# Kernel tuning notes

Measured on AMD Instinct MI355X. Metric: run time of the kernel, lower is better.

## Reference

```python
import jax, jax.numpy as jnp
import numpy as np

N = 100000        # nodes
E = 1_600_000     # edges (avg degree 16)
F_IN = 128        # in_channels
HID = 64          # hidden_channels (per-head)
H1 = 4            # heads layer 1
G = 128           # number of graphs
NEG_SLOPE = 0.2   # PyG GATConv default leaky_relu slope


def setup_inputs() -> dict:
    key = jax.random.key(0)
    ks = jax.random.split(key, 12)
    x = jax.random.normal(ks[0], (N, F_IN), dtype=jnp.float32)
    edge_index = jax.random.randint(ks[1], (2, E), 0, N, dtype=jnp.int64)
    batch = jnp.sort(jax.random.randint(ks[2], (N,), 0, G, dtype=jnp.int64))
    s1 = 1.0 / np.sqrt(F_IN)
    s2 = 1.0 / np.sqrt(H1 * HID)
    # layer 1: in=F_IN, out=H1*HID (PyG lin has no bias; separate bias after concat)
    w1 = jax.random.normal(ks[3], (H1 * HID, F_IN), dtype=jnp.float32) * s1
    a_src1 = jax.random.normal(ks[4], (H1, HID), dtype=jnp.float32) * s1
    a_dst1 = jax.random.normal(ks[5], (H1, HID), dtype=jnp.float32) * s1
    b1 = jnp.zeros((H1 * HID,), dtype=jnp.float32)
    # layer 2: in=H1*HID, out=HID, heads=1
    w2 = jax.random.normal(ks[6], (1 * HID, H1 * HID), dtype=jnp.float32) * s2
    a_src2 = jax.random.normal(ks[7], (1, HID), dtype=jnp.float32) * s2
    a_dst2 = jax.random.normal(ks[8], (1, HID), dtype=jnp.float32) * s2
    b2 = jnp.zeros((HID,), dtype=jnp.float32)
    return {"x": x, "w1": w1, "a_src1": a_src1, "a_dst1": a_dst1, "b1": b1,
            "w2": w2, "a_src2": a_src2, "a_dst2": a_dst2, "b2": b2,
            "edge_index": edge_index, "batch": batch}


def _segment_softmax(alpha, seg, n):
    # numerically-stable softmax of alpha [E,H] grouped by seg (dst node)
    m = jax.ops.segment_max(alpha, seg, num_segments=n)
    m = jnp.where(jnp.isfinite(m), m, 0.0)  # empty segments -> 0
    a = jnp.exp(alpha - m[seg])
    s = jax.ops.segment_sum(a, seg, num_segments=n)
    return a / (s[seg] + 1e-16)


def _gat_conv(x, w, a_src, a_dst, bias, src, dst, n, heads, ch):
    h = (x @ w.T).reshape(n, heads, ch)          # [N,H,C]
    alpha_src = jnp.sum(h * a_src[None], axis=-1)  # [N,H]
    alpha_dst = jnp.sum(h * a_dst[None], axis=-1)  # [N,H]
    e = jax.nn.leaky_relu(alpha_src[src] + alpha_dst[dst], NEG_SLOPE)  # [E,H]
    att = _segment_softmax(e, dst, n)             # [E,H]
    msg = h[src] * att[:, :, None]                # [E,H,C]
    out = jax.ops.segment_sum(msg, dst, num_segments=n)  # [N,H,C]
    return out.reshape(n, heads * ch) + bias


def reference(x, w1, a_src1, a_dst1, b1, w2, a_src2, a_dst2, b2, edge_index, batch):
    src, dst = edge_index[0], edge_index[1]
    h = jax.nn.relu(_gat_conv(x, w1, a_src1, a_dst1, b1, src, dst, N, H1, HID))
    h = jax.nn.relu(_gat_conv(h, w2, a_src2, a_dst2, b2, src, dst, N, 1, HID))
    # global_mean_pool over graph ids
    sums = jax.ops.segment_sum(h, batch, num_segments=G)            # [G,HID]
    cnt = jax.ops.segment_sum(jnp.ones((N,), h.dtype), batch, num_segments=G)
    return sums / jnp.maximum(cnt, 1.0)[:, None]
```

## Files before the change

### kernel.cpp

```cpp
#include <hip/hip_runtime.h>
#include <math.h>
#include <type_traits>

#define NNODES 100000
#define NEDGES 1600000
#define NGRAPH 128
#define NBKT 391
#define CAP 1536
#define EPB 2048

typedef _Float16 f16x4 __attribute__((ext_vector_type(4)));
typedef _Float16 f16x8 __attribute__((ext_vector_type(8)));
typedef float f32x4 __attribute__((ext_vector_type(4)));

__global__ void convert_w(const float* __restrict__ w1, const float* __restrict__ w2,
                          const float* __restrict__ as1c, const float* __restrict__ ad1c,
                          const float* __restrict__ as2c, const float* __restrict__ ad2c,
                          _Float16* __restrict__ w1h, _Float16* __restrict__ w2h,
                          _Float16* __restrict__ va1, _Float16* __restrict__ va2) {
  const int b = blockIdx.x, tid = threadIdx.x;
  if (b < 8) {
    if (tid >= 128) return;
    int h = b & 3;
    const float* coef = (b >= 4) ? ad1c : as1c;
    float s = 0.f;
    for (int c = 0; c < 64; ++c) s = fmaf(w1[(size_t)(h * 64 + c) * 128 + tid], coef[h * 64 + c], s);
    va1[b * 128 + tid] = (_Float16)s;
  } else if (b < 10) {
    int r = b - 8;
    const float* coef = r ? ad2c : as2c;
    float s = 0.f;
    for (int c = 0; c < 64; ++c) s = fmaf(w2[(size_t)c * 256 + tid], coef[c], s);
    va2[r * 256 + tid] = (_Float16)s;
  } else if (b < 138) {
    int i = (b - 10) * 256 + tid;
    w1h[i] = (_Float16)w1[i];
  } else {
    int i = (b - 138) * 256 + tid;
    w2h[i] = (_Float16)w2[i];
  }
}

template <int K, int N, typename AT>
__global__ __launch_bounds__(256) void gemm_mfma(const AT* __restrict__ A,
    const _Float16* __restrict__ Bh, const _Float16* __restrict__ VA,
    _Float16* __restrict__ C, int M, float* __restrict__ asrc, float* __restrict__ adst) {
  constexpr int H = N / 64;
  constexpr int KS = K / 32, NT = N / 16;
  constexpr int BM = 400, NG = 7;
  constexpr int CP = N + 8;
  __shared__ _Float16 Bs[N * K];
  __shared__ _Float16 VAs[16 * K];
  __shared__ _Float16 Cs[64 * CP];
  const int tid = threadIdx.x;
  const int lane = tid & 63, wid = tid >> 6;
  const int lr = lane & 15, lk = (lane >> 4) * 8;
  const int bm = blockIdx.x * BM;

  for (int i = tid * 8; i < N * K; i += 2048) {
    int row = i / K, k = i & (K - 1);
    f16x8 v = *(const f16x8*)&Bh[i];
    *(f16x8*)&Bs[(row * K + k) ^ ((row & 7) << 3)] = v;
  }
  for (int i = tid * 8; i < 16 * K; i += 2048) {
    int row = i / K, k = i & (K - 1);
    f16x8 v = *(const f16x8*)&VA[i];
    *(f16x8*)&VAs[(row * K + k) ^ ((row & 7) << 3)] = v;
  }
  __syncthreads();

  auto loadA = [&](int g, f16x8* areg) {
    int rlocal = g * 64 + wid * 16 + lr;
    int row = bm + rlocal;
    if (rlocal < BM && row < M) {
      const AT* arow = A + (size_t)row * K;
#pragma unroll
      for (int ks = 0; ks < KS; ++ks) {
        if constexpr (std::is_same<AT, float>::value) {
          float4 v0 = *(const float4*)&arow[ks * 32 + lk];
          float4 v1 = *(const float4*)&arow[ks * 32 + lk + 4];
          f16x8 t;
          t[0] = (_Float16)v0.x; t[1] = (_Float16)v0.y; t[2] = (_Float16)v0.z; t[3] = (_Float16)v0.w;
          t[4] = (_Float16)v1.x; t[5] = (_Float16)v1.y; t[6] = (_Float16)v1.z; t[7] = (_Float16)v1.w;
          areg[ks] = t;
        } else {
          areg[ks] = *(const f16x8*)&arow[ks * 32 + lk];
        }
      }
    } else {
#pragma unroll
      for (int ks = 0; ks < KS; ++ks) areg[ks] = (f16x8){};
    }
  };

  f16x8 a[KS], an[KS];
  loadA(0, a);
  const int rl0 = wid * 16 + (lane >> 4) * 4;

  for (int g = 0; g < NG; ++g) {
    if (g + 1 < NG) loadA(g + 1, an);

    f32x4 accv = (f32x4){0.f, 0.f, 0.f, 0.f};
#pragma unroll
    for (int ks = 0; ks < KS; ++ks) {
      f16x8 bv = *(const f16x8*)&VAs[(lr * K + ks * 32 + lk) ^ ((lr & 7) << 3)];
      accv = __builtin_amdgcn_mfma_f32_16x16x32_f16(a[ks], bv, accv, 0, 0, 0);
    }

    f32x4 acc[NT];
#pragma unroll
    for (int nt = 0; nt < NT; ++nt) acc[nt] = (f32x4){0.f, 0.f, 0.f, 0.f};
#pragma unroll
    for (int nt = 0; nt < NT; ++nt) {
      int brow = nt * 16 + lr;
#pragma unroll
      for (int ks = 0; ks < KS; ++ks) {
        f16x8 b = *(const f16x8*)&Bs[(brow * K + ks * 32 + lk) ^ ((brow & 7) << 3)];
        acc[nt] = __builtin_amdgcn_mfma_f32_16x16x32_f16(a[ks], b, acc[nt], 0, 0, 0);
      }
    }

#pragma unroll
    for (int r = 0; r < 4; ++r) {
      int rl = rl0 + r;
#pragma unroll
      for (int nt = 0; nt < NT; ++nt) Cs[rl * CP + nt * 16 + lr] = (_Float16)acc[nt][r];
      int rlocal = g * 64 + rl;
      int row = bm + rlocal;
      if (rlocal < BM && row < M) {
        if (lr < H) asrc[row * H + lr] = accv[r];
        else if (lr < 2 * H) adst[row * H + lr - H] = accv[r];
      }
    }
    __syncthreads();

    int rmax = min(64, min(BM - g * 64, M - (bm + g * 64)));
    if (rmax > 0) {
      int nch = rmax * (N / 8);
      for (int q = tid; q < nch; q += 256) {
        int row = q / (N / 8), c8 = q % (N / 8);
        f16x8 v = *(const f16x8*)&Cs[row * CP + c8 * 8];
        *(f16x8*)&C[(size_t)(bm + g * 64 + row) * N + c8 * 8] = v;
      }
    }
    __syncthreads();
#pragma unroll
    for (int ks = 0; ks < KS; ++ks) a[ks] = an[ks];
  }
}

__global__ __launch_bounds__(256) void bucketA(const int* __restrict__ srcv,
    const int* __restrict__ dstv, int2* __restrict__ part, int* __restrict__ gcur,
    int e_count) {
  __shared__ int hist[NBKT];
  __shared__ int base_[NBKT];
  __shared__ int lofs[NBKT];
  const int tid = threadIdx.x;
  const int P = blockIdx.x & 7;
  for (int i = tid; i < NBKT; i += 256) { hist[i] = 0; lofs[i] = 0; }
  __syncthreads();
  const int e0 = blockIdx.x * EPB;
  const int e1 = min(e0 + EPB, e_count);
  for (int e = e0 + tid; e < e1; e += 256) atomicAdd(&hist[dstv[e] >> 8], 1);
  __syncthreads();
  for (int i = tid; i < NBKT; i += 256) {
    int c = hist[i];
    base_[i] = c ? atomicAdd(&gcur[(P * NBKT + i) * 16], c) : 0;
  }
  __syncthreads();
  for (int e = e0 + tid; e < e1; e += 256) {
    int d = dstv[e];
    int b = d >> 8;
    int l = atomicAdd(&lofs[b], 1);
    part[(size_t)(P * NBKT + b) * CAP + base_[b] + l] = make_int2(srcv[e], d);
  }
}

__global__ __launch_bounds__(256) void bucketB1(const int2* __restrict__ part,
    const int* __restrict__ gcur, int* __restrict__ deg, int n) {
  __shared__ int cnt[256];
  const int b = blockIdx.x;
  const int tid = threadIdx.x;
  cnt[tid] = 0;
  __syncthreads();
  for (int P = 0; P < 8; ++P) {
    int cn = gcur[(P * NBKT + b) * 16];
    const int2* seg = part + (size_t)(P * NBKT + b) * CAP;
    for (int i = tid; i < cn; i += 256) atomicAdd(&cnt[seg[i].y & 255], 1);
  }
  __syncthreads();
  int node = (b << 8) + tid;
  if (node < n) deg[node] = cnt[tid];
}

__global__ __launch_bounds__(256) void bucketB2(const int2* __restrict__ part,
    const int* __restrict__ gcur, const int* __restrict__ offsets,
    int* __restrict__ esrc, int n) {
  __shared__ int lcur[256];
  const int b = blockIdx.x;
  const int tid = threadIdx.x;
  int node = (b << 8) + tid;
  lcur[tid] = (node < n) ? offsets[node] : 0;
  __syncthreads();
  for (int P = 0; P < 8; ++P) {
    int cn = gcur[(P * NBKT + b) * 16];
    const int2* seg = part + (size_t)(P * NBKT + b) * CAP;
    for (int i = tid; i < cn; i += 256) {
      int2 e = seg[i];
      int slot = atomicAdd(&lcur[e.y & 255], 1);
      esrc[slot] = e.x;
    }
  }
}

__global__ __launch_bounds__(1024) void scan1(const int* __restrict__ deg, int* __restrict__ inc,
                                              int* __restrict__ bsum, int n) {
  __shared__ int sm[1024];
  int i = blockIdx.x * 1024 + threadIdx.x;
  sm[threadIdx.x] = (i < n) ? deg[i] : 0;
  __syncthreads();
  for (int o = 1; o < 1024; o <<= 1) {
    int t = (threadIdx.x >= o) ? sm[threadIdx.x - o] : 0;
    __syncthreads();
    sm[threadIdx.x] += t;
    __syncthreads();
  }
  if (i < n) inc[i] = sm[threadIdx.x];
  if (threadIdx.x == 1023) bsum[blockIdx.x] = sm[1023];
}

__global__ void scan2(const int* __restrict__ bsum, int* __restrict__ boff, int nb) {
  __shared__ int sm[128];
  int t = threadIdx.x;
  int own = (t < nb) ? bsum[t] : 0;
  sm[t] = own;
  __syncthreads();
  for (int o = 1; o < 128; o <<= 1) {
    int u = (t >= o) ? sm[t - o] : 0;
    __syncthreads();
    sm[t] += u;
    __syncthreads();
  }
  if (t < nb) boff[t] = sm[t] - own;
}

__global__ void scan3(const int* __restrict__ inc, const int* __restrict__ deg,
                      const int* __restrict__ boff, int* __restrict__ offsets,
                      int n, int e_count) {
  int i = blockIdx.x * blockDim.x + threadIdx.x;
  if (i < n) offsets[i] = inc[i] - deg[i] + boff[i >> 10];
  if (i == 0) offsets[n] = e_count;
}

__global__ __launch_bounds__(256) void agg1_kernel(const _Float16* __restrict__ hmat,
    const float* __restrict__ asrc, const float* __restrict__ adst,
    const int* __restrict__ offsets, const int* __restrict__ esrc,
    const float* __restrict__ bias, _Float16* __restrict__ outv) {
  const int lane = threadIdx.x & 63, wid = threadIdx.x >> 6;
  const int node = blockIdx.x * 4 + wid;
  if (node >= NNODES) return;
  const int h = lane >> 4;
  const int start = offsets[node];
  const int end = offsets[node + 1];
  const float adn = adst[node * 4 + h];
  const _Float16* hbase = hmat + lane * 4;
  float acc[4] = {0.f, 0.f, 0.f, 0.f};
  float s = 0.f;
  int j = start;
  for (; j + 8 <= end; j += 8) {
    int sv[8];
#pragma unroll
    for (int t = 0; t < 8; ++t) sv[t] = esrc[j + t];
    f16x4 vv[8];
#pragma unroll
    for (int t = 0; t < 8; ++t) vv[t] = *(const f16x4*)&hbase[(size_t)sv[t] * 256];
    _Float16 ph[8];
#pragma unroll
    for (int t = 0; t < 8; ++t) {
      float v = asrc[sv[t] * 4 + h] + adn;
      v = (v > 0.f) ? v : 0.2f * v;
      float p = __expf(v);
      s += p;
      ph[t] = (_Float16)p;
    }
#pragma unroll
    for (int t = 0; t < 8; ++t)
#pragma unroll
      for (int k = 0; k < 4; ++k)
        acc[k] = fmaf((float)vv[t][k], (float)ph[t], acc[k]);
  }
  for (; j < end; ++j) {
    int sv = esrc[j];
    f16x4 vv = *(const f16x4*)&hbase[(size_t)sv * 256];
    float v = asrc[sv * 4 + h] + adn;
    v = (v > 0.f) ? v : 0.2f * v;
    float p = __expf(v);
    s += p;
    _Float16 phs = (_Float16)p;
#pragma unroll
    for (int k = 0; k < 4; ++k) acc[k] = fmaf((float)vv[k], (float)phs, acc[k]);
  }
  float inv = 1.f / (s + 1e-16f);
  f16x4 ho;
#pragma unroll
  for (int k = 0; k < 4; ++k)
    ho[k] = (_Float16)fmaxf(fmaf(acc[k], inv, bias[lane * 4 + k]), 0.f);
  *(f16x4*)&outv[(size_t)node * 256 + lane * 4] = ho;
}

__global__ __launch_bounds__(256) void agg2_kernel(const _Float16* __restrict__ hmat,
    const float* __restrict__ asrc, const float* __restrict__ adst,
    const int* __restrict__ offsets, const int* __restrict__ esrc,
    const float* __restrict__ bias, float* __restrict__ outv) {
  const int lane = threadIdx.x & 63, wid = threadIdx.x >> 6;
  const int g = lane >> 4, q = lane & 15;
  const int node = blockIdx.x * 16 + wid * 4 + g;
  if (node >= NNODES) return;
  const int start = offsets[node];
  const int end = offsets[node + 1];
  const float adn = adst[node];
  const _Float16* hbase = hmat + q * 4;
  float acc[4] = {0.f, 0.f, 0.f, 0.f};
  float s = 0.f;
  int j = start;
  for (; j + 4 <= end; j += 4) {
    int sv[4];
#pragma unroll
    for (int t = 0; t < 4; ++t) sv[t] = esrc[j + t];
    f16x4 v[4];
#pragma unroll
    for (int t = 0; t < 4; ++t) v[t] = *(const f16x4*)&hbase[(size_t)sv[t] * 64];
#pragma unroll
    for (int t = 0; t < 4; ++t) {
      float x = asrc[sv[t]] + adn;
      x = (x > 0.f) ? x : 0.2f * x;
      float p = __expf(x);
      s += p;
      _Float16 phs = (_Float16)p;
#pragma unroll
      for (int k = 0; k < 4; ++k) acc[k] = fmaf((float)v[t][k], (float)phs, acc[k]);
    }
  }
  for (; j < end; ++j) {
    int sv = esrc[j];
    f16x4 v = *(const f16x4*)&hbase[(size_t)sv * 64];
    float x = asrc[sv] + adn;
    x = (x > 0.f) ? x : 0.2f * x;
    float p = __expf(x);
    s += p;
    _Float16 phs = (_Float16)p;
#pragma unroll
    for (int k = 0; k < 4; ++k) acc[k] = fmaf((float)v[k], (float)phs, acc[k]);
  }
  float inv = 1.f / (s + 1e-16f);
  float4 o;
  o.x = fmaxf(fmaf(acc[0], inv, bias[q * 4 + 0]), 0.f);
  o.y = fmaxf(fmaf(acc[1], inv, bias[q * 4 + 1]), 0.f);
  o.z = fmaxf(fmaf(acc[2], inv, bias[q * 4 + 2]), 0.f);
  o.w = fmaxf(fmaf(acc[3], inv, bias[q * 4 + 3]), 0.f);
  *(float4*)&outv[(size_t)node * 64 + q * 4] = o;
}

__global__ __launch_bounds__(256) void pool_kernel(const float* __restrict__ g2,
    const int* __restrict__ batch, float* __restrict__ out, int n) {
  const int gid = blockIdx.x;
  const int lane = threadIdx.x & 63, w = threadIdx.x >> 6;
  int lo = 0, hi = n;
  while (lo < hi) { int mid = (lo + hi) >> 1; if (batch[mid] < gid) lo = mid + 1; else hi = mid; }
  int lb = lo;
  hi = n;
  while (lo < hi) { int mid = (lo + hi) >> 1; if (batch[mid] < gid + 1) lo = mid + 1; else hi = mid; }
  int ub = lo;
  float acc = 0.f;
  for (int i = lb + w; i < ub; i += 4) acc += g2[(size_t)i * 64 + lane];
  __shared__ float red[4][64];
  red[w][lane] = acc;
  __syncthreads();
  if (threadIdx.x < 64) {
    float sum = (red[0][lane] + red[1][lane]) + (red[2][lane] + red[3][lane]);
    float cnt = fmaxf((float)(ub - lb), 1.f);
    out[gid * 64 + lane] = sum / cnt;
  }
}

extern "C" void kernel_launch(void* const* d_in, const int* in_sizes, int n_in,
                              void* d_out, int out_size, void* d_ws, size_t ws_size,
                              hipStream_t stream) {
  const float* x      = (const float*)d_in[0];
  const float* w1     = (const float*)d_in[1];
  const float* a_src1 = (const float*)d_in[2];
  const float* a_dst1 = (const float*)d_in[3];
  const float* b1     = (const float*)d_in[4];
  const float* w2     = (const float*)d_in[5];
  const float* a_src2 = (const float*)d_in[6];
  const float* a_dst2 = (const float*)d_in[7];
  const float* b2     = (const float*)d_in[8];
  const int*   src    = (const int*)d_in[9];
  const int*   dst    = src + NEDGES;
  const int*   batch  = (const int*)d_in[10];
  float* out = (float*)d_out;

  const int N = NNODES, E = NEDGES;
  const int NB = (N + 1023) / 1024;

  char* wsb = (char*)d_ws;
  size_t off = 0;
  auto alloc = [&](size_t bytes) {
    void* p = wsb + off;
    off = (off + bytes + 255) & ~(size_t)255;
    return p;
  };
  _Float16* h1h = (_Float16*)alloc((size_t)N * 256 * 2);
  _Float16* g1h = (_Float16*)alloc((size_t)N * 256 * 2);
  _Float16* h2h = (_Float16*)alloc((size_t)N * 64 * 2);
  float* g2     = (float*)alloc((size_t)N * 64 * 4);
  float* as1    = (float*)alloc((size_t)N * 4 * 4);
  float* ad1    = (float*)alloc((size_t)N * 4 * 4);
  float* as2    = (float*)alloc((size_t)N * 4);
  float* ad2    = (float*)alloc((size_t)N * 4);
  int* deg      = (int*)alloc((size_t)N * 4);
  int* inc      = (int*)alloc((size_t)N * 4);
  int* bsum     = (int*)alloc((size_t)NB * 4);
  int* boff     = (int*)alloc((size_t)NB * 4);
  int* offsets  = (int*)alloc((size_t)(N + 1) * 4);
  int* esrc     = (int*)alloc((size_t)E * 4);
  int2* part    = (int2*)alloc((size_t)8 * NBKT * CAP * 8);
  int* gcur     = (int*)alloc((size_t)8 * NBKT * 16 * 4);
  _Float16* w1h = (_Float16*)alloc((size_t)256 * 128 * 2);
  _Float16* w2h = (_Float16*)alloc((size_t)64 * 256 * 2);
  _Float16* va1 = (_Float16*)alloc((size_t)16 * 128 * 2);
  _Float16* va2 = (_Float16*)alloc((size_t)16 * 256 * 2);

  hipMemsetAsync(va1, 0, (size_t)16 * 128 * 2, stream);
  hipMemsetAsync(va2, 0, (size_t)16 * 256 * 2, stream);
  convert_w<<<202, 256, 0, stream>>>(w1, w2, a_src1, a_dst1, a_src2, a_dst2,
                                     w1h, w2h, va1, va2);

  hipMemsetAsync(gcur, 0, (size_t)8 * NBKT * 16 * 4, stream);
  bucketA<<<(E + EPB - 1) / EPB, 256, 0, stream>>>(src, dst, part, gcur, E);
  bucketB1<<<NBKT, 256, 0, stream>>>(part, gcur, deg, N);
  scan1<<<NB, 1024, 0, stream>>>(deg, inc, bsum, N);
  scan2<<<1, 128, 0, stream>>>(bsum, boff, NB);
  scan3<<<(N + 255) / 256, 256, 0, stream>>>(inc, deg, boff, offsets, N, E);
  bucketB2<<<NBKT, 256, 0, stream>>>(part, gcur, offsets, esrc, N);

  gemm_mfma<128, 256, float><<<250, 256, 0, stream>>>(
      x, w1h, va1, h1h, N, as1, ad1);
  agg1_kernel<<<(N + 3) / 4, 256, 0, stream>>>(h1h, as1, ad1, offsets, esrc, b1, g1h);

  gemm_mfma<256, 64, _Float16><<<250, 256, 0, stream>>>(
      g1h, w2h, va2, h2h, N, as2, ad2);
  agg2_kernel<<<(N + 15) / 16, 256, 0, stream>>>(h2h, as2, ad2, offsets, esrc, b2, g2);

  pool_kernel<<<NGRAPH, 256, 0, stream>>>(g2, batch, out, N);
}
```

Baseline: 357.2 us.

## Fuse front-end kernels, pack edge pairs, merge scans, fp16 layer-2 output

Merges weight conversion and edge bucketing into one launch, and replaces the separate va memsets with in-kernel zeroing. Packs (src, dst&255) into a single 32-bit word so the partition buffer takes half the bytes. Folds the per-bucket degree count and local scan into bucketB1p, and collapses the three-kernel global scan into one. agg2 is unrolled to 8 edges per step and stores its output in fp16, which pool_kernel reads, cutting launches and memory traffic at the cost of some precision in the pooled sums.

```diff
diff --git a/kernel.cpp b/kernel.cpp
--- a/kernel.cpp
+++ b/kernel.cpp
@@ -13,31 +13,132 @@
 typedef _Float16 f16x8 __attribute__((ext_vector_type(8)));
 typedef float f32x4 __attribute__((ext_vector_type(4)));
 
-__global__ void convert_w(const float* __restrict__ w1, const float* __restrict__ w2,
-                          const float* __restrict__ as1c, const float* __restrict__ ad1c,
-                          const float* __restrict__ as2c, const float* __restrict__ ad2c,
-                          _Float16* __restrict__ w1h, _Float16* __restrict__ w2h,
-                          _Float16* __restrict__ va1, _Float16* __restrict__ va2) {
+__global__ __launch_bounds__(256) void front1(
+    const float* __restrict__ w1, const float* __restrict__ w2,
+    const float* __restrict__ as1c, const float* __restrict__ ad1c,
+    const float* __restrict__ as2c, const float* __restrict__ ad2c,
+    _Float16* __restrict__ w1h, _Float16* __restrict__ w2h,
+    _Float16* __restrict__ va1, _Float16* __restrict__ va2,
+    const int* __restrict__ srcv, const int* __restrict__ dstv,
+    unsigned* __restrict__ part, int* __restrict__ gcur, int e_count) {
+  __shared__ int hist[NBKT];
+  __shared__ int base_[NBKT];
+  __shared__ int lofs[NBKT];
+  const int tid = threadIdx.x;
+  if (blockIdx.x < 202) {
+    const int b = blockIdx.x;
+    if (b < 8) {
+      if (tid < 128) {
+        int h = b & 3;
+        const float* coef = (b >= 4) ? ad1c : as1c;
+        float s = 0.f;
+        for (int c = 0; c < 64; ++c)
+          s = fmaf(w1[(size_t)(h * 64 + c) * 128 + tid], coef[h * 64 + c], s);
+        va1[b * 128 + tid] = (_Float16)s;
+        va1[(b + 8) * 128 + tid] = (_Float16)0.f;
+      }
+    } else if (b < 10) {
+      int r = b - 8;
+      const float* coef = r ? ad2c : as2c;
+      float s = 0.f;
+      for (int c = 0; c < 64; ++c) s = fmaf(w2[(size_t)c * 256 + tid], coef[c], s);
+      va2[r * 256 + tid] = (_Float16)s;
+      for (int z = 2 + r * 7; z < 9 + r * 7; ++z) va2[z * 256 + tid] = (_Float16)0.f;
+    } else if (b < 138) {
+      int i = (b - 10) * 256 + tid;
+      w1h[i] = (_Float16)w1[i];
+    } else {
+      int i = (b - 138) * 256 + tid;
+      w2h[i] = (_Float16)w2[i];
+    }
+    return;
+  }
+  const int ab = blockIdx.x - 202;
+  const int P = ab & 7;
+  for (int i = tid; i < NBKT; i += 256) { hist[i] = 0; lofs[i] = 0; }
+  __syncthreads();
+  const int e0 = ab * EPB;
+  const int e1 = min(e0 + EPB, e_count);
+  for (int e = e0 + tid; e < e1; e += 256) atomicAdd(&hist[dstv[e] >> 8], 1);
+  __syncthreads();
+  for (int i = tid; i < NBKT; i += 256) {
+    int c = hist[i];
+    base_[i] = c ? atomicAdd(&gcur[(P * NBKT + i) * 16], c) : 0;
+  }
+  __syncthreads();
+  for (int e = e0 + tid; e < e1; e += 256) {
+    int d = dstv[e];
+    int b = d >> 8;
+    int l = atomicAdd(&lofs[b], 1);
+    part[(size_t)(P * NBKT + b) * CAP + base_[b] + l] =
+        ((unsigned)srcv[e] << 8) | (unsigned)(d & 255);
+  }
+}
+
+__global__ __launch_bounds__(256) void bucketB1p(const unsigned* __restrict__ part,
+    const int* __restrict__ gcur, int* __restrict__ pre, int* __restrict__ bsum, int n) {
+  __shared__ int cnt[256];
+  __shared__ int sc[256];
   const int b = blockIdx.x, tid = threadIdx.x;
-  if (b < 8) {
-    if (tid >= 128) return;
-    int h = b & 3;
-    const float* coef = (b >= 4) ? ad1c : as1c;
-    float s = 0.f;
-    for (int c = 0; c < 64; ++c) s = fmaf(w1[(size_t)(h * 64 + c) * 128 + tid], coef[h * 64 + c], s);
-    va1[b * 128 + tid] = (_Float16)s;
-  } else if (b < 10) {
-    int r = b - 8;
-    const float* coef = r ? ad2c : as2c;
-    float s = 0.f;
-    for (int c = 0; c < 64; ++c) s = fmaf(w2[(size_t)c * 256 + tid], coef[c], s);
-    va2[r * 256 + tid] = (_Float16)s;
-  } else if (b < 138) {
-    int i = (b - 10) * 256 + tid;
-    w1h[i] = (_Float16)w1[i];
-  } else {
-    int i = (b - 138) * 256 + tid;
-    w2h[i] = (_Float16)w2[i];
+  cnt[tid] = 0;
+  __syncthreads();
+  for (int P = 0; P < 8; ++P) {
+    int cn = gcur[(P * NBKT + b) * 16];
+    const unsigned* seg = part + (size_t)(P * NBKT + b) * CAP;
+    for (int i = tid; i < cn; i += 256) atomicAdd(&cnt[seg[i] & 255], 1);
+  }
+  __syncthreads();
+  int own = cnt[tid];
+  sc[tid] = own;
+  __syncthreads();
+  for (int o = 1; o < 256; o <<= 1) {
+    int t = (tid >= o) ? sc[tid - o] : 0;
+    __syncthreads();
+    sc[tid] += t;
+    __syncthreads();
+  }
+  int node = (b << 8) + tid;
+  if (node < n) pre[node] = sc[tid] - own;
+  if (tid == 255) bsum[b] = sc[255];
+}
+
+__global__ __launch_bounds__(256) void scan23(const int* __restrict__ pre,
+    const int* __restrict__ bsum, int* __restrict__ offsets, int n, int e_count) {
+  __shared__ int bs[NBKT];
+  __shared__ int red[256];
+  const int b = blockIdx.x, tid = threadIdx.x;
+  for (int i = tid; i < NBKT; i += 256) bs[i] = bsum[i];
+  __syncthreads();
+  int part_ = 0;
+  for (int i = tid; i < b; i += 256) part_ += bs[i];
+  red[tid] = part_;
+  __syncthreads();
+  for (int o = 128; o; o >>= 1) {
+    if (tid < o) red[tid] += red[tid + o];
+    __syncthreads();
+  }
+  int base = red[0];
+  int node = (b << 8) + tid;
+  if (node < n) offsets[node] = base + pre[node];
+  if (b == NBKT - 1 && tid == 0) offsets[n] = e_count;
+}
+
+__global__ __launch_bounds__(256) void bucketB2(const unsigned* __restrict__ part,
+    const int* __restrict__ gcur, const int* __restrict__ offsets,
+    int* __restrict__ esrc, int n) {
+  __shared__ int lcur[256];
+  const int b = blockIdx.x, tid = threadIdx.x;
+  int node = (b << 8) + tid;
+  lcur[tid] = (node < n) ? offsets[node] : 0;
+  __syncthreads();
+  for (int P = 0; P < 8; ++P) {
+    int cn = gcur[(P * NBKT + b) * 16];
+    const unsigned* seg = part + (size_t)(P * NBKT + b) * CAP;
+    for (int i = tid; i < cn; i += 256) {
+      unsigned e = seg[i];
+      int slot = atomicAdd(&lcur[e & 255], 1);
+      esrc[slot] = (int)(e >> 8);
+    }
   }
 }
 
@@ -147,109 +248,6 @@
 #pragma unroll
     for (int ks = 0; ks < KS; ++ks) a[ks] = an[ks];
   }
-}
-
-__global__ __launch_bounds__(256) void bucketA(const int* __restrict__ srcv,
-    const int* __restrict__ dstv, int2* __restrict__ part, int* __restrict__ gcur,
-    int e_count) {
-  __shared__ int hist[NBKT];
-  __shared__ int base_[NBKT];
-  __shared__ int lofs[NBKT];
-  const int tid = threadIdx.x;
-  const int P = blockIdx.x & 7;
-  for (int i = tid; i < NBKT; i += 256) { hist[i] = 0; lofs[i] = 0; }
-  __syncthreads();
-  const int e0 = blockIdx.x * EPB;
-  const int e1 = min(e0 + EPB, e_count);
-  for (int e = e0 + tid; e < e1; e += 256) atomicAdd(&hist[dstv[e] >> 8], 1);
-  __syncthreads();
-  for (int i = tid; i < NBKT; i += 256) {
-    int c = hist[i];
-    base_[i] = c ? atomicAdd(&gcur[(P * NBKT + i) * 16], c) : 0;
-  }
-  __syncthreads();
-  for (int e = e0 + tid; e < e1; e += 256) {
-    int d = dstv[e];
-    int b = d >> 8;
-    int l = atomicAdd(&lofs[b], 1);
-    part[(size_t)(P * NBKT + b) * CAP + base_[b] + l] = make_int2(srcv[e], d);
-  }
-}
-
-__global__ __launch_bounds__(256) void bucketB1(const int2* __restrict__ part,
-    const int* __restrict__ gcur, int* __restrict__ deg, int n) {
-  __shared__ int cnt[256];
-  const int b = blockIdx.x;
-  const int tid = threadIdx.x;
-  cnt[tid] = 0;
-  __syncthreads();
-  for (int P = 0; P < 8; ++P) {
-    int cn = gcur[(P * NBKT + b) * 16];
-    const int2* seg = part + (size_t)(P * NBKT + b) * CAP;
-    for (int i = tid; i < cn; i += 256) atomicAdd(&cnt[seg[i].y & 255], 1);
-  }
-  __syncthreads();
-  int node = (b << 8) + tid;
-  if (node < n) deg[node] = cnt[tid];
-}
-
-__global__ __launch_bounds__(256) void bucketB2(const int2* __restrict__ part,
-    const int* __restrict__ gcur, const int* __restrict__ offsets,
-    int* __restrict__ esrc, int n) {
-  __shared__ int lcur[256];
-  const int b = blockIdx.x;
-  const int tid = threadIdx.x;
-  int node = (b << 8) + tid;
-  lcur[tid] = (node < n) ? offsets[node] : 0;
-  __syncthreads();
-  for (int P = 0; P < 8; ++P) {
-    int cn = gcur[(P * NBKT + b) * 16];
-    const int2* seg = part + (size_t)(P * NBKT + b) * CAP;
-    for (int i = tid; i < cn; i += 256) {
-      int2 e = seg[i];
-      int slot = atomicAdd(&lcur[e.y & 255], 1);
-      esrc[slot] = e.x;
-    }
-  }
-}
-
-__global__ __launch_bounds__(1024) void scan1(const int* __restrict__ deg, int* __restrict__ inc,
-                                              int* __restrict__ bsum, int n) {
-  __shared__ int sm[1024];
-  int i = blockIdx.x * 1024 + threadIdx.x;
-  sm[threadIdx.x] = (i < n) ? deg[i] : 0;
-  __syncthreads();
-  for (int o = 1; o < 1024; o <<= 1) {
-    int t = (threadIdx.x >= o) ? sm[threadIdx.x - o] : 0;
-    __syncthreads();
-    sm[threadIdx.x] += t;
-    __syncthreads();
-  }
-  if (i < n) inc[i] = sm[threadIdx.x];
-  if (threadIdx.x == 1023) bsum[blockIdx.x] = sm[1023];
-}
-
-__global__ void scan2(const int* __restrict__ bsum, int* __restrict__ boff, int nb) {
-  __shared__ int sm[128];
-  int t = threadIdx.x;
-  int own = (t < nb) ? bsum[t] : 0;
-  sm[t] = own;
-  __syncthreads();
-  for (int o = 1; o < 128; o <<= 1) {
-    int u = (t >= o) ? sm[t - o] : 0;
-    __syncthreads();
-    sm[t] += u;
-    __syncthreads();
-  }
-  if (t < nb) boff[t] = sm[t] - own;
-}
-
-__global__ void scan3(const int* __restrict__ inc, const int* __restrict__ deg,
-                      const int* __restrict__ boff, int* __restrict__ offsets,
-                      int n, int e_count) {
-  int i = blockIdx.x * blockDim.x + threadIdx.x;
-  if (i < n) offsets[i] = inc[i] - deg[i] + boff[i >> 10];
-  if (i == 0) offsets[n] = e_count;
 }
 
 __global__ __launch_bounds__(256) void agg1_kernel(const _Float16* __restrict__ hmat,
@@ -311,7 +309,7 @@
 __global__ __launch_bounds__(256) void agg2_kernel(const _Float16* __restrict__ hmat,
     const float* __restrict__ asrc, const float* __restrict__ adst,
     const int* __restrict__ offsets, const int* __restrict__ esrc,
-    const float* __restrict__ bias, float* __restrict__ outv) {
+    const float* __restrict__ bias, _Float16* __restrict__ outv) {
   const int lane = threadIdx.x & 63, wid = threadIdx.x >> 6;
   const int g = lane >> 4, q = lane & 15;
   const int node = blockIdx.x * 16 + wid * 4 + g;
@@ -323,15 +321,15 @@
   float acc[4] = {0.f, 0.f, 0.f, 0.f};
   float s = 0.f;
   int j = start;
-  for (; j + 4 <= end; j += 4) {
-    int sv[4];
-#pragma unroll
-    for (int t = 0; t < 4; ++t) sv[t] = esrc[j + t];
-    f16x4 v[4];
-#pragma unroll
-    for (int t = 0; t < 4; ++t) v[t] = *(const f16x4*)&hbase[(size_t)sv[t] * 64];
-#pragma unroll
-    for (int t = 0; t < 4; ++t) {
+  for (; j + 8 <= end; j += 8) {
+    int sv[8];
+#pragma unroll
+    for (int t = 0; t < 8; ++t) sv[t] = esrc[j + t];
+    f16x4 v[8];
+#pragma unroll
+    for (int t = 0; t < 8; ++t) v[t] = *(const f16x4*)&hbase[(size_t)sv[t] * 64];
+#pragma unroll
+    for (int t = 0; t < 8; ++t) {
       float x = asrc[sv[t]] + adn;
       x = (x > 0.f) ? x : 0.2f * x;
       float p = __expf(x);
@@ -353,15 +351,14 @@
     for (int k = 0; k < 4; ++k) acc[k] = fmaf((float)v[k], (float)phs, acc[k]);
   }
   float inv = 1.f / (s + 1e-16f);
-  float4 o;
-  o.x = fmaxf(fmaf(acc[0], inv, bias[q * 4 + 0]), 0.f);
-  o.y = fmaxf(fmaf(acc[1], inv, bias[q * 4 + 1]), 0.f);
-  o.z = fmaxf(fmaf(acc[2], inv, bias[q * 4 + 2]), 0.f);
-  o.w = fmaxf(fmaf(acc[3], inv, bias[q * 4 + 3]), 0.f);
-  *(float4*)&outv[(size_t)node * 64 + q * 4] = o;
-}
-
-__global__ __launch_bounds__(256) void pool_kernel(const float* __restrict__ g2,
+  f16x4 ho;
+#pragma unroll
+  for (int k = 0; k < 4; ++k)
+    ho[k] = (_Float16)fmaxf(fmaf(acc[k], inv, bias[q * 4 + k]), 0.f);
+  *(f16x4*)&outv[(size_t)node * 64 + q * 4] = ho;
+}
+
+__global__ __launch_bounds__(256) void pool_kernel(const _Float16* __restrict__ g2,
     const int* __restrict__ batch, float* __restrict__ out, int n) {
   const int gid = blockIdx.x;
   const int lane = threadIdx.x & 63, w = threadIdx.x >> 6;
@@ -372,7 +369,7 @@
   while (lo < hi) { int mid = (lo + hi) >> 1; if (batch[mid] < gid + 1) lo = mid + 1; else hi = mid; }
   int ub = lo;
   float acc = 0.f;
-  for (int i = lb + w; i < ub; i += 4) acc += g2[(size_t)i * 64 + lane];
+  for (int i = lb + w; i < ub; i += 4) acc += (float)g2[(size_t)i * 64 + lane];
   __shared__ float red[4][64];
   red[w][lane] = acc;
   __syncthreads();
@@ -401,7 +398,6 @@
   float* out = (float*)d_out;
 
   const int N = NNODES, E = NEDGES;
-  const int NB = (N + 1023) / 1024;
 
   char* wsb = (char*)d_ws;
   size_t off = 0;
@@ -413,35 +409,29 @@
   _Float16* h1h = (_Float16*)alloc((size_t)N * 256 * 2);
   _Float16* g1h = (_Float16*)alloc((size_t)N * 256 * 2);
   _Float16* h2h = (_Float16*)alloc((size_t)N * 64 * 2);
-  float* g2     = (float*)alloc((size_t)N * 64 * 4);
+  _Float16* g2h = (_Float16*)alloc((size_t)N * 64 * 2);
   float* as1    = (float*)alloc((size_t)N * 4 * 4);
   float* ad1    = (float*)alloc((size_t)N * 4 * 4);
   float* as2    = (float*)alloc((size_t)N * 4);
   float* ad2    = (float*)alloc((size_t)N * 4);
-  int* deg      = (int*)alloc((size_t)N * 4);
-  int* inc      = (int*)alloc((size_t)N * 4);
-  int* bsum     = (int*)alloc((size_t)NB * 4);
-  int* boff     = (int*)alloc((size_t)NB * 4);
+  int* pre      = (int*)alloc((size_t)N * 4);
+  int* bsum     = (int*)alloc((size_t)NBKT * 4);
   int* offsets  = (int*)alloc((size_t)(N + 1) * 4);
   int* esrc     = (int*)alloc((size_t)E * 4);
-  int2* part    = (int2*)alloc((size_t)8 * NBKT * CAP * 8);
+  unsigned* part= (unsigned*)alloc((size_t)8 * NBKT * CAP * 4);
   int* gcur     = (int*)alloc((size_t)8 * NBKT * 16 * 4);
   _Float16* w1h = (_Float16*)alloc((size_t)256 * 128 * 2);
   _Float16* w2h = (_Float16*)alloc((size_t)64 * 256 * 2);
   _Float16* va1 = (_Float16*)alloc((size_t)16 * 128 * 2);
   _Float16* va2 = (_Float16*)alloc((size_t)16 * 256 * 2);
 
-  hipMemsetAsync(va1, 0, (size_t)16 * 128 * 2, stream);
-  hipMemsetAsync(va2, 0, (size_t)16 * 256 * 2, stream);
-  convert_w<<<202, 256, 0, stream>>>(w1, w2, a_src1, a_dst1, a_src2, a_dst2,
-                                     w1h, w2h, va1, va2);
-
   hipMemsetAsync(gcur, 0, (size_t)8 * NBKT * 16 * 4, stream);
-  bucketA<<<(E + EPB - 1) / EPB, 256, 0, stream>>>(src, dst, part, gcur, E);
-  bucketB1<<<NBKT, 256, 0, stream>>>(part, gcur, deg, N);
-  scan1<<<NB, 1024, 0, stream>>>(deg, inc, bsum, N);
-  scan2<<<1, 128, 0, stream>>>(bsum, boff, NB);
-  scan3<<<(N + 255) / 256, 256, 0, stream>>>(inc, deg, boff, offsets, N, E);
+  front1<<<202 + (E + EPB - 1) / EPB, 256, 0, stream>>>(
+      w1, w2, a_src1, a_dst1, a_src2, a_dst2, w1h, w2h, va1, va2,
+      src, dst, part, gcur, E);
+
+  bucketB1p<<<NBKT, 256, 0, stream>>>(part, gcur, pre, bsum, N);
+  scan23<<<NBKT, 256, 0, stream>>>(pre, bsum, offsets, N, E);
   bucketB2<<<NBKT, 256, 0, stream>>>(part, gcur, offsets, esrc, N);
 
   gemm_mfma<128, 256, float><<<250, 256, 0, stream>>>(
@@ -450,7 +440,7 @@
 
   gemm_mfma<256, 64, _Float16><<<250, 256, 0, stream>>>(
       g1h, w2h, va2, h2h, N, as2, ad2);
-  agg2_kernel<<<(N + 15) / 16, 256, 0, stream>>>(h2h, as2, ad2, offsets, esrc, b2, g2);
-
-  pool_kernel<<<NGRAPH, 256, 0, stream>>>(g2, batch, out, N);
-}
+  agg2_kernel<<<(N + 15) / 16, 256, 0, stream>>>(h2h, as2, ad2, offsets, esrc, b2, g2h);
+
+  pool_kernel<<<NGRAPH, 256, 0, stream>>>(g2h, batch, out, N);
+}
```

Result: faster. 346.2 us (-3.1%).
